# Optimization experiments

Hardware: AMD Instinct MI355X
Metric: run time of the kernel (lower is better)

The kernel has to match this reference:

```python
import jax, jax.numpy as jnp
import numpy as np

B, IN, H, O, L, G = 4096, 512, 1024, 256, 2, 3


def _lin_init(key, out_dim, in_dim):
    k1, k2 = jax.random.split(key)
    bound = 1.0 / np.sqrt(in_dim)
    w = jax.random.uniform(k1, (out_dim, in_dim), jnp.float32, -bound, bound)
    b = jax.random.uniform(k2, (out_dim,), jnp.float32, -bound, bound)
    return w, b


def setup_inputs() -> dict:
    key = jax.random.key(0)
    ks = jax.random.split(key, 10)
    x = jax.random.normal(ks[0], (B, IN), jnp.float32)
    hidden = jax.random.normal(ks[1], (L, B, H), jnp.float32)
    i2d_w, i2d_b = _lin_init(ks[2], H, IN)
    # stacked GRU params, PyTorch gate order (r, z, n); layer0 input dim == H (after i2d)
    kih = jax.random.split(ks[3], L)
    khh = jax.random.split(ks[4], L)
    gru_w_ih = jnp.stack([_lin_init(kih[l], 3 * H, H)[0] for l in range(L)])
    gru_b_ih = jnp.stack([_lin_init(kih[l], 3 * H, H)[1] for l in range(L)])
    gru_w_hh = jnp.stack([_lin_init(khh[l], 3 * H, H)[0] for l in range(L)])
    gru_b_hh = jnp.stack([_lin_init(khh[l], 3 * H, H)[1] for l in range(L)])
    mu_w, mu_b = _lin_init(ks[5], O * G, H)
    sigma_w, sigma_b = _lin_init(ks[6], O * G, H)
    pi_w, pi_b = _lin_init(ks[7], O * G, H)
    return {"x": x, "hidden": hidden, "i2d_w": i2d_w, "i2d_b": i2d_b,
            "gru_w_ih": gru_w_ih, "gru_w_hh": gru_w_hh,
            "gru_b_ih": gru_b_ih, "gru_b_hh": gru_b_hh,
            "mu_w": mu_w, "mu_b": mu_b, "sigma_w": sigma_w, "sigma_b": sigma_b,
            "pi_w": pi_w, "pi_b": pi_b, "batch_size": B}


def reference(x, hidden, i2d_w, i2d_b, gru_w_ih, gru_w_hh, gru_b_ih, gru_b_hh,
              mu_w, mu_b, sigma_w, sigma_b, pi_w, pi_b, batch_size):
    # input projection + relu
    h1 = jax.nn.relu(x @ i2d_w.T + i2d_b)  # [B, H]
    # single-timestep stacked GRU (PyTorch cell math, gate order r,z,n)
    inp = h1
    new_h = []
    for l in range(hidden.shape[0]):
        h_prev = hidden[l]
        gi = inp @ gru_w_ih[l].T + gru_b_ih[l]   # [B, 3H]
        gh = h_prev @ gru_w_hh[l].T + gru_b_hh[l]
        i_r, i_z, i_n = jnp.split(gi, 3, axis=-1)
        h_r, h_z, h_n = jnp.split(gh, 3, axis=-1)
        r = jax.nn.sigmoid(i_r + h_r)
        z = jax.nn.sigmoid(i_z + h_z)
        n = jnp.tanh(i_n + r * h_n)
        h_new = (1.0 - z) * n + z * h_prev
        new_h.append(h_new)
        inp = h_new
    hidden_out = jnp.stack(new_h)            # [L, B, H]
    h_out = jnp.tanh(inp)                    # [B, H]
    n_g = 3
    o = mu_w.shape[0] // n_g
    pi = jax.nn.softmax((h_out @ pi_w.T + pi_b).reshape(-1, n_g, o), axis=1)
    mu = (h_out @ mu_w.T + mu_b).reshape(-1, n_g, o)
    sig = jax.nn.softplus(h_out @ sigma_w.T + sigma_b).reshape(-1, n_g, o)
    return (mu, sig, pi, hidden_out)
```

## Files before the change

### kernel.cpp

```cpp
#include <hip/hip_runtime.h>
#include <stdint.h>

typedef unsigned short bf16u;
typedef float f32x4 __attribute__((ext_vector_type(4)));
typedef short bf16x8 __attribute__((ext_vector_type(8)));
typedef float f4 __attribute__((ext_vector_type(4)));

#define AS1 __attribute__((address_space(1)))
#define AS3 __attribute__((address_space(3)))

__device__ __forceinline__ float b2f(bf16u u) {
  union { uint32_t i; float f; } v; v.i = ((uint32_t)u) << 16; return v.f;
}
__device__ __forceinline__ uint32_t f2b(float f) {
  union { float f; uint32_t i; } v; v.f = f;
  uint32_t i = v.i;
  return (i + 0x7FFFu + ((i >> 16) & 1u)) >> 16;
}
__device__ __forceinline__ float sigm(float x) { return 1.f / (1.f + __expf(-x)); }
__device__ __forceinline__ float ftanh(float x) {
  float e = __expf(2.f * x);
  return 1.f - 2.f / (e + 1.f);
}
__device__ __forceinline__ uint4 pack8(f4 a, f4 b) {
  uint4 o;
  o.x = (f2b(a[0]) & 0xffffu) | (f2b(a[1]) << 16);
  o.y = (f2b(a[2]) & 0xffffu) | (f2b(a[3]) << 16);
  o.z = (f2b(b[0]) & 0xffffu) | (f2b(b[1]) << 16);
  o.w = (f2b(b[2]) & 0xffffu) | (f2b(b[3]) << 16);
  return o;
}

struct CvtSeg { const float* src; char* dst; int blk0; int count; int tobf16; };
struct CvtArgs { CvtSeg s[12]; int nseg; };

__global__ __launch_bounds__(256)
void cvt_multi(CvtArgs a) {
  int b = blockIdx.x, seg = 0;
  while (seg + 1 < a.nseg && b >= a.s[seg + 1].blk0) ++seg;
  const CvtSeg& S = a.s[seg];
  size_t idx = ((size_t)(b - S.blk0) * 2048) + (size_t)threadIdx.x * 8;
  if ((long long)idx >= S.count) return;
  f4 x = *(const f4*)&S.src[idx];
  f4 y = *(const f4*)&S.src[idx + 4];
  if (S.tobf16) {
    *(uint4*)((bf16u*)S.dst + idx) = pack8(x, y);
  } else {
    *(f4*)((float*)S.dst + idx) = x;
    *(f4*)((float*)S.dst + idx + 4) = y;
  }
}

__global__ __launch_bounds__(256)
void gemm_i2d(const float* __restrict__ xf, const bf16u* __restrict__ W,
              const float* __restrict__ bias, bf16u* __restrict__ Cout) {
  constexpr int K = 512, N = 1024;
  __shared__ bf16u sA[64 * 64];
  __shared__ bf16u sB[128 * 64];
  const int tid = threadIdx.x, wave = tid >> 6, lane = tid & 63;
  const int bn = blockIdx.x, bm = blockIdx.y;

  const int srA = wave * 16 + (lane >> 3);
  const int srB = wave * 32 + (lane >> 3);
  const int kc  = (lane & 7) ^ ((lane >> 3) & 7);
  const float* gx = xf + (size_t)(bm * 64 + srA) * K + kc * 8;
  const bf16u* wg = W + (size_t)(bn * 128 + srB) * K + kc * 8;
  const int adst = srA * 64 + (lane & 7) * 8;

  const int wm = wave >> 1, wn = wave & 1;
  const int q = lane >> 4, cl = lane & 15;

  int aoff[2][2], boff[4][2];
#pragma unroll
  for (int i = 0; i < 2; ++i) {
    int m = wm * 32 + i * 16 + cl;
#pragma unroll
    for (int kk = 0; kk < 2; ++kk)
      aoff[i][kk] = m * 64 + (((q + kk * 4) ^ (m & 7)) * 8);
  }
#pragma unroll
  for (int j = 0; j < 4; ++j) {
    int n = wn * 64 + j * 16 + cl;
#pragma unroll
    for (int kk = 0; kk < 2; ++kk)
      boff[j][kk] = n * 64 + (((q + kk * 4) ^ (n & 7)) * 8);
  }

  f32x4 acc[2][4] = {};
  for (int k0 = 0; k0 < K; k0 += 64) {
    f4 a0 = *(const f4*)(gx + k0);
    f4 a1 = *(const f4*)(gx + k0 + 4);
    f4 a2 = *(const f4*)(gx + (size_t)8 * K + k0);
    f4 a3 = *(const f4*)(gx + (size_t)8 * K + k0 + 4);
#pragma unroll
    for (int t = 0; t < 4; ++t)
      __builtin_amdgcn_global_load_lds(
          (const AS1 void*)(wg + k0 + (size_t)t * 8 * K),
          (AS3 void*)&sB[wave * 2048 + t * 512], 16, 0, 0);
    *(uint4*)&sA[adst]       = pack8(a0, a1);
    *(uint4*)&sA[adst + 512] = pack8(a2, a3);
    __syncthreads();
#pragma unroll
    for (int kk = 0; kk < 2; ++kk) {
      bf16x8 af[2], bfr[4];
#pragma unroll
      for (int i = 0; i < 2; ++i) af[i] = *(const bf16x8*)&sA[aoff[i][kk]];
#pragma unroll
      for (int j = 0; j < 4; ++j) bfr[j] = *(const bf16x8*)&sB[boff[j][kk]];
#pragma unroll
      for (int i = 0; i < 2; ++i)
#pragma unroll
        for (int j = 0; j < 4; ++j)
          acc[i][j] = __builtin_amdgcn_mfma_f32_16x16x32_bf16(af[i], bfr[j], acc[i][j], 0, 0, 0);
    }
    __syncthreads();
  }

  float bv[4];
#pragma unroll
  for (int j = 0; j < 4; ++j)
    bv[j] = bias[bn * 128 + wn * 64 + j * 16 + cl];

  const int row0 = bm * 64 + wm * 32 + q * 4;
  const int col0 = bn * 128 + wn * 64 + cl;
#pragma unroll
  for (int i = 0; i < 2; ++i)
#pragma unroll
    for (int j = 0; j < 4; ++j)
#pragma unroll
      for (int r = 0; r < 4; ++r) {
        float v = fmaxf(acc[i][j][r] + bv[j], 0.f);
        Cout[(size_t)(row0 + i * 16 + r) * N + (col0 + j * 16)] = (bf16u)f2b(v);
      }
}

template <int LAST>
__global__ __launch_bounds__(512)
void gru_fused(const bf16u* __restrict__ inp, const bf16u* __restrict__ hpb,
               const bf16u* __restrict__ wih, const bf16u* __restrict__ whh,
               const float* __restrict__ bih, const float* __restrict__ bhh,
               const float* __restrict__ hpf, float* __restrict__ hid_out,
               bf16u* __restrict__ nxt) {
  constexpr int K = 1024;
  __shared__ bf16u s[640 * 64];
  const int tid  = threadIdx.x;
  const int wave = tid >> 6;
  const int lane = tid & 63;
  const int bn = blockIdx.x, bm = blockIdx.y;
  const int c0 = bn * 64;

  const int rr  = tid >> 3;
  const int kc  = (tid & 7) ^ (rr & 7);
  const int dst0 = rr * 64 + (tid & 7) * 8;
  const bf16u* gI = inp + (size_t)(bm * 128 + rr) * K + kc * 8;
  const bf16u* gH = hpb + (size_t)(bm * 128 + rr) * K + kc * 8;
  const bf16u* gW[6];
#pragma unroll
  for (int p = 0; p < 6; ++p) {
    const bf16u* base = (p < 3) ? wih : whh;
    gW[p] = base + (size_t)((p % 3) * 1024 + c0 + rr) * K + kc * 8;
  }

  const int wm = wave >> 1, wn = wave & 1;
  const int q = lane >> 4, cl = lane & 15;

  int aoff[2][2], boff[2][2];
#pragma unroll
  for (int i = 0; i < 2; ++i) {
    int ai = wm * 32 + i * 16 + cl;
#pragma unroll
    for (int kk = 0; kk < 2; ++kk)
      aoff[i][kk] = ai * 64 + (((q + kk * 4) ^ (ai & 7)) * 8);
  }
#pragma unroll
  for (int j = 0; j < 2; ++j) {
    int br = wn * 32 + j * 16 + cl;
#pragma unroll
    for (int kk = 0; kk < 2; ++kk)
      boff[j][kk] = (256 + br) * 64 + (((q + kk * 4) ^ (br & 7)) * 8);
  }

  f32x4 acc[6][2][2] = {};

  for (int k0 = 0; k0 < K; k0 += 64) {
    __builtin_amdgcn_global_load_lds((const AS1 void*)(gI + k0),
        (AS3 void*)&s[dst0], 16, 0, 0);
    __builtin_amdgcn_global_load_lds((const AS1 void*)(gI + k0 + (size_t)64 * K),
        (AS3 void*)&s[dst0 + 4096], 16, 0, 0);
    __builtin_amdgcn_global_load_lds((const AS1 void*)(gH + k0),
        (AS3 void*)&s[dst0 + 8192], 16, 0, 0);
    __builtin_amdgcn_global_load_lds((const AS1 void*)(gH + k0 + (size_t)64 * K),
        (AS3 void*)&s[dst0 + 12288], 16, 0, 0);
#pragma unroll
    for (int p = 0; p < 6; ++p)
      __builtin_amdgcn_global_load_lds((const AS1 void*)(gW[p] + k0),
          (AS3 void*)&s[dst0 + (4 + p) * 4096], 16, 0, 0);
    __syncthreads();
#pragma unroll
    for (int kk = 0; kk < 2; ++kk) {
      bf16x8 aI[2], aH[2];
#pragma unroll
      for (int i = 0; i < 2; ++i) {
        aI[i] = *(const bf16x8*)&s[aoff[i][kk]];
        aH[i] = *(const bf16x8*)&s[aoff[i][kk] + 8192];
      }
#pragma unroll
      for (int p = 0; p < 6; ++p) {
        bf16x8 b0 = *(const bf16x8*)&s[boff[0][kk] + p * 4096];
        bf16x8 b1 = *(const bf16x8*)&s[boff[1][kk] + p * 4096];
        if (p < 3) {
          acc[p][0][0] = __builtin_amdgcn_mfma_f32_16x16x32_bf16(aI[0], b0, acc[p][0][0], 0, 0, 0);
          acc[p][0][1] = __builtin_amdgcn_mfma_f32_16x16x32_bf16(aI[0], b1, acc[p][0][1], 0, 0, 0);
          acc[p][1][0] = __builtin_amdgcn_mfma_f32_16x16x32_bf16(aI[1], b0, acc[p][1][0], 0, 0, 0);
          acc[p][1][1] = __builtin_amdgcn_mfma_f32_16x16x32_bf16(aI[1], b1, acc[p][1][1], 0, 0, 0);
        } else {
          acc[p][0][0] = __builtin_amdgcn_mfma_f32_16x16x32_bf16(aH[0], b0, acc[p][0][0], 0, 0, 0);
          acc[p][0][1] = __builtin_amdgcn_mfma_f32_16x16x32_bf16(aH[0], b1, acc[p][0][1], 0, 0, 0);
          acc[p][1][0] = __builtin_amdgcn_mfma_f32_16x16x32_bf16(aH[1], b0, acc[p][1][0], 0, 0, 0);
          acc[p][1][1] = __builtin_amdgcn_mfma_f32_16x16x32_bf16(aH[1], b1, acc[p][1][1], 0, 0, 0);
        }
      }
    }
    __syncthreads();
  }

  float bI[3][2], bH[3][2];
#pragma unroll
  for (int g = 0; g < 3; ++g)
#pragma unroll
    for (int j = 0; j < 2; ++j) {
      int col = c0 + wn * 32 + j * 16 + cl;
      bI[g][j] = bih[g * 1024 + col];
      bH[g][j] = bhh[g * 1024 + col];
    }

#pragma unroll
  for (int i = 0; i < 2; ++i)
#pragma unroll
    for (int j = 0; j < 2; ++j)
#pragma unroll
      for (int r_ = 0; r_ < 4; ++r_) {
        int row = bm * 128 + wm * 32 + i * 16 + q * 4 + r_;
        int col = c0 + wn * 32 + j * 16 + cl;
        size_t o = (size_t)row * 1024 + col;
        float vir = acc[0][i][j][r_] + bI[0][j];
        float viz = acc[1][i][j][r_] + bI[1][j];
        float vin = acc[2][i][j][r_] + bI[2][j];
        float vhr = acc[3][i][j][r_] + bH[0][j];
        float vhz = acc[4][i][j][r_] + bH[1][j];
        float vhn = acc[5][i][j][r_] + bH[2][j];
        float rg = sigm(vir + vhr);
        float zg = sigm(viz + vhz);
        float ng = ftanh(vin + rg * vhn);
        float hnew = (1.f - zg) * ng + zg * hpf[o];
        hid_out[o] = hnew;
        nxt[o] = (bf16u)f2b(LAST ? ftanh(hnew) : hnew);
      }
}

__global__ __launch_bounds__(256)
void gemm_heads2(const bf16u* __restrict__ A, const bf16u* __restrict__ Wp,
                 const float* __restrict__ biasp, float* __restrict__ out_mu,
                 float* __restrict__ out_sg, float* __restrict__ out_pi) {
  constexpr int K = 1024;
  __shared__ bf16u sA[64 * 64];
  __shared__ bf16u sB[192 * 64];
  const int tid = threadIdx.x, wave = tid >> 6, lane = tid & 63;
  const int bn = blockIdx.x, bm = blockIdx.y;
  const bool ispi = (bn >= 12);
  const int o0 = (bn - 12) * 64;
  const int nbt = ispi ? 6 : 4;

  const int srA = wave * 16 + (lane >> 3);
  const int kc  = (lane & 7) ^ ((lane >> 3) & 7);
  const bf16u* ag = A + (size_t)(bm * 64 + srA) * K + kc * 8;
  const bf16u* wg[6];
#pragma unroll
  for (int t = 0; t < 6; ++t) {
    int wrow;
    if (!ispi) wrow = bn * 128 + t * 32 + wave * 8 + (lane >> 3);
    else       wrow = 1536 + (t >> 1) * 256 + o0 + (t & 1) * 32 + wave * 8 + (lane >> 3);
    wg[t] = Wp + (size_t)wrow * K + kc * 8;
  }

  const int wm = wave >> 1, wn = wave & 1;
  const int q = lane >> 4, cl = lane & 15;

  int aoff[2][2], boff[6][2];
#pragma unroll
  for (int i = 0; i < 2; ++i) {
    int m = wm * 32 + i * 16 + cl;
#pragma unroll
    for (int kk = 0; kk < 2; ++kk)
      aoff[i][kk] = m * 64 + (((q + kk * 4) ^ (m & 7)) * 8);
  }
#pragma unroll
  for (int j = 0; j < 6; ++j) {
    int l = ispi ? ((j >> 1) * 64 + wn * 32 + (j & 1) * 16 + cl)
                 : (wn * 64 + (j & 3) * 16 + cl);
#pragma unroll
    for (int kk = 0; kk < 2; ++kk)
      boff[j][kk] = l * 64 + (((q + kk * 4) ^ (l & 7)) * 8);
  }

  f32x4 acc[2][6] = {};
  for (int k0 = 0; k0 < K; k0 += 64) {
#pragma unroll
    for (int t = 0; t < 2; ++t)
      __builtin_amdgcn_global_load_lds(
          (const AS1 void*)(ag + k0 + (size_t)t * 8 * K),
          (AS3 void*)&sA[wave * 1024 + t * 512], 16, 0, 0);
#pragma unroll
    for (int t = 0; t < 6; ++t)
      if (t < nbt)
        __builtin_amdgcn_global_load_lds(
            (const AS1 void*)(wg[t] + k0),
            (AS3 void*)&sB[t * 2048 + wave * 512], 16, 0, 0);
    __syncthreads();
#pragma unroll
    for (int kk = 0; kk < 2; ++kk) {
      bf16x8 af[2];
#pragma unroll
      for (int i = 0; i < 2; ++i) af[i] = *(const bf16x8*)&sA[aoff[i][kk]];
#pragma unroll
      for (int j = 0; j < 6; ++j) {
        if (j >= nbt) continue;
        bf16x8 bf_ = *(const bf16x8*)&sB[boff[j][kk]];
#pragma unroll
        for (int i = 0; i < 2; ++i)
          acc[i][j] = __builtin_amdgcn_mfma_f32_16x16x32_bf16(af[i], bf_, acc[i][j], 0, 0, 0);
      }
    }
    __syncthreads();
  }

  const int row0 = bm * 64 + wm * 32 + q * 4;
  if (!ispi) {
    float bv[4];
#pragma unroll
    for (int j = 0; j < 4; ++j)
      bv[j] = biasp[bn * 128 + wn * 64 + j * 16 + cl];
    const int head = bn / 6;
    const int ch0 = (bn % 6) * 128 + wn * 64 + cl;
#pragma unroll
    for (int i = 0; i < 2; ++i)
#pragma unroll
      for (int j = 0; j < 4; ++j)
#pragma unroll
        for (int r = 0; r < 4; ++r) {
          float v = acc[i][j][r] + bv[j];
          size_t off = (size_t)(row0 + i * 16 + r) * 768 + (ch0 + j * 16);
          if (head == 0) out_mu[off] = v;
          else out_sg[off] = fmaxf(v, 0.f) + __logf(1.f + __expf(-fabsf(v)));
        }
  } else {
    float bv[6];
#pragma unroll
    for (int j = 0; j < 6; ++j)
      bv[j] = biasp[1536 + (j >> 1) * 256 + o0 + wn * 32 + (j & 1) * 16 + cl];
#pragma unroll
    for (int i = 0; i < 2; ++i)
#pragma unroll
      for (int jo = 0; jo < 2; ++jo)
#pragma unroll
        for (int r = 0; r < 4; ++r) {
          float v0 = acc[i][jo][r]     + bv[jo];
          float v1 = acc[i][2 + jo][r] + bv[2 + jo];
          float v2 = acc[i][4 + jo][r] + bv[4 + jo];
          float m = fmaxf(fmaxf(v0, v1), v2);
          float e0 = __expf(v0 - m), e1 = __expf(v1 - m), e2 = __expf(v2 - m);
          float sc = 1.f / (e0 + e1 + e2);
          size_t base = (size_t)(row0 + i * 16 + r) * 768
                        + (o0 + wn * 32 + jo * 16 + cl);
          out_pi[base]       = e0 * sc;
          out_pi[base + 256] = e1 * sc;
          out_pi[base + 512] = e2 * sc;
        }
  }
}

extern "C" void kernel_launch(void* const* d_in, const int* in_sizes, int n_in,
                              void* d_out, int out_size, void* d_ws, size_t ws_size,
                              hipStream_t stream) {
  const float* x      = (const float*)d_in[0];
  const float* hidden = (const float*)d_in[1];
  const float* i2d_w  = (const float*)d_in[2];
  const float* i2d_b  = (const float*)d_in[3];
  const float* w_ih   = (const float*)d_in[4];
  const float* w_hh   = (const float*)d_in[5];
  const float* b_ih   = (const float*)d_in[6];
  const float* b_hh   = (const float*)d_in[7];
  const float* mu_w   = (const float*)d_in[8];
  const float* mu_b   = (const float*)d_in[9];
  const float* sg_w   = (const float*)d_in[10];
  const float* sg_b   = (const float*)d_in[11];
  const float* pi_w   = (const float*)d_in[12];
  const float* pi_b   = (const float*)d_in[13];
  float* out = (float*)d_out;

  const size_t BH = 4194304;
  const int HS = 3145728;
  float* hid_base = out + (size_t)3 * HS;

  dim3 blk(256, 1, 1);

  bf16u* wb_i2d = (bf16u*)d_ws;
  bf16u* wb_ih  = wb_i2d + 524288;
  bf16u* wb_hh  = wb_ih + 6291456;
  bf16u* wb_hd  = wb_hh + 6291456;
  float* biasp  = (float*)((char*)d_ws + 30932992);
  const size_t wbytes = 30942208;

  {
    CvtArgs a{};
    int nb = 0;
    auto seg = [&](const float* s, void* d, int count, int tobf) {
      a.s[a.nseg++] = {s, (char*)d, nb, count, tobf};
      nb += (count + 2047) / 2048;
    };
    seg(i2d_w, wb_i2d, 524288, 1);
    seg(w_ih,  wb_ih, 6291456, 1);
    seg(w_hh,  wb_hh, 6291456, 1);
    seg(mu_w,  wb_hd, 786432, 1);
    seg(sg_w,  wb_hd + 786432, 786432, 1);
    seg(pi_w,  wb_hd + 1572864, 786432, 1);
    seg(mu_b,  biasp, 768, 0);
    seg(sg_b,  biasp + 768, 768, 0);
    seg(pi_b,  biasp + 1536, 768, 0);
    cvt_multi<<<dim3(nb), blk, 0, stream>>>(a);
  }

  int Bc = 4096;
  while (wbytes + (size_t)Bc * 8192 > ws_size && Bc > 256) Bc >>= 1;
  const int nchunk = 4096 / Bc;

  char* cbase = (char*)d_ws + wbytes;
  bf16u* ws0  = (bf16u*)cbase;
  bf16u* nxt0 = (bf16u*)(cbase + (size_t)Bc * 2048);
  bf16u* hb0  = (bf16u*)(cbase + (size_t)Bc * 4096);
  bf16u* hb1  = (bf16u*)(cbase + (size_t)Bc * 6144);

  for (int c = 0; c < nchunk; ++c) {
    const size_t off = (size_t)c * Bc;
    const float* h0_c = hidden + off * 1024;
    const float* h1_c = hidden + BH + off * 1024;

    {
      CvtArgs a{};
      int nb = 0;
      auto seg = [&](const float* s, void* d, int count) {
        a.s[a.nseg++] = {s, (char*)d, nb, count, 1};
        nb += (count + 2047) / 2048;
      };
      seg(h0_c, hb0, Bc * 1024);
      seg(h1_c, hb1, Bc * 1024);
      cvt_multi<<<dim3(nb), blk, 0, stream>>>(a);
    }

    gemm_i2d<<<dim3(8, Bc / 64), blk, 0, stream>>>(
        x + off * 512, wb_i2d, i2d_b, ws0);
    gru_fused<0><<<dim3(16, Bc / 128), dim3(512, 1, 1), 0, stream>>>(
        ws0, hb0, wb_ih, wb_hh, b_ih, b_hh, h0_c, hid_base + off * 1024, nxt0);
    gru_fused<1><<<dim3(16, Bc / 128), dim3(512, 1, 1), 0, stream>>>(
        nxt0, hb1, wb_ih + 3145728, wb_hh + 3145728, b_ih + 3072, b_hh + 3072,
        h1_c, hid_base + BH + off * 1024, ws0);
    gemm_heads2<<<dim3(16, Bc / 64), blk, 0, stream>>>(
        ws0, wb_hd, biasp, out + off * 768, out + HS + off * 768,
        out + 2 * (size_t)HS + off * 768);
  }
}
```

Measured before the change: 367.2 us.

## Merge hidden-state conversion into weight conversion and widen heads GEMM tile

The hidden-state fp32-to-bf16 conversion is folded into the single upfront weight conversion launch, so it is no longer a separate per-chunk launch. The workspace layout is reorganized to hold the full bf16 hidden buffers. The heads GEMM now uses 512-thread blocks covering 128 rows with one shared LDS buffer, which halves the grid and lets each B tile be reused across more rows. The risks are larger LDS use per block, possible occupancy loss, and a bigger workspace requirement that may shrink the chunk size.

```diff
diff --git a/kernel.cpp b/kernel.cpp
--- a/kernel.cpp
+++ b/kernel.cpp
@@ -258,29 +258,28 @@
       }
 }
 
-__global__ __launch_bounds__(256)
-void gemm_heads2(const bf16u* __restrict__ A, const bf16u* __restrict__ Wp,
+__global__ __launch_bounds__(512)
+void gemm_heads3(const bf16u* __restrict__ A, const bf16u* __restrict__ Wp,
                  const float* __restrict__ biasp, float* __restrict__ out_mu,
                  float* __restrict__ out_sg, float* __restrict__ out_pi) {
   constexpr int K = 1024;
-  __shared__ bf16u sA[64 * 64];
-  __shared__ bf16u sB[192 * 64];
+  __shared__ bf16u s[320 * 64];
   const int tid = threadIdx.x, wave = tid >> 6, lane = tid & 63;
   const int bn = blockIdx.x, bm = blockIdx.y;
   const bool ispi = (bn >= 12);
   const int o0 = (bn - 12) * 64;
-  const int nbt = ispi ? 6 : 4;
-
-  const int srA = wave * 16 + (lane >> 3);
-  const int kc  = (lane & 7) ^ ((lane >> 3) & 7);
-  const bf16u* ag = A + (size_t)(bm * 64 + srA) * K + kc * 8;
-  const bf16u* wg[6];
-#pragma unroll
-  for (int t = 0; t < 6; ++t) {
-    int wrow;
-    if (!ispi) wrow = bn * 128 + t * 32 + wave * 8 + (lane >> 3);
-    else       wrow = 1536 + (t >> 1) * 256 + o0 + (t & 1) * 32 + wave * 8 + (lane >> 3);
-    wg[t] = Wp + (size_t)wrow * K + kc * 8;
+  const int nbt = ispi ? 3 : 2;
+  const int nj  = ispi ? 6 : 4;
+
+  const int rr  = tid >> 3;
+  const int kc  = (tid & 7) ^ (rr & 7);
+  const int dst0 = rr * 64 + (tid & 7) * 8;
+  const bf16u* gA = A + (size_t)(bm * 128 + rr) * K + kc * 8;
+  const bf16u* gB[3];
+#pragma unroll
+  for (int t = 0; t < 3; ++t) {
+    int wrow = ispi ? (1536 + t * 256 + o0 + rr) : (bn * 128 + t * 64 + rr);
+    gB[t] = Wp + (size_t)wrow * K + kc * 8;
   }
 
   const int wm = wave >> 1, wn = wave & 1;
@@ -300,32 +299,30 @@
                  : (wn * 64 + (j & 3) * 16 + cl);
 #pragma unroll
     for (int kk = 0; kk < 2; ++kk)
-      boff[j][kk] = l * 64 + (((q + kk * 4) ^ (l & 7)) * 8);
+      boff[j][kk] = 8192 + l * 64 + (((q + kk * 4) ^ (l & 7)) * 8);
   }
 
   f32x4 acc[2][6] = {};
   for (int k0 = 0; k0 < K; k0 += 64) {
-#pragma unroll
-    for (int t = 0; t < 2; ++t)
-      __builtin_amdgcn_global_load_lds(
-          (const AS1 void*)(ag + k0 + (size_t)t * 8 * K),
-          (AS3 void*)&sA[wave * 1024 + t * 512], 16, 0, 0);
-#pragma unroll
-    for (int t = 0; t < 6; ++t)
+    __builtin_amdgcn_global_load_lds((const AS1 void*)(gA + k0),
+        (AS3 void*)&s[dst0], 16, 0, 0);
+    __builtin_amdgcn_global_load_lds((const AS1 void*)(gA + k0 + (size_t)64 * K),
+        (AS3 void*)&s[dst0 + 4096], 16, 0, 0);
+#pragma unroll
+    for (int t = 0; t < 3; ++t)
       if (t < nbt)
-        __builtin_amdgcn_global_load_lds(
-            (const AS1 void*)(wg[t] + k0),
-            (AS3 void*)&sB[t * 2048 + wave * 512], 16, 0, 0);
+        __builtin_amdgcn_global_load_lds((const AS1 void*)(gB[t] + k0),
+            (AS3 void*)&s[8192 + dst0 + t * 4096], 16, 0, 0);
     __syncthreads();
 #pragma unroll
     for (int kk = 0; kk < 2; ++kk) {
       bf16x8 af[2];
 #pragma unroll
-      for (int i = 0; i < 2; ++i) af[i] = *(const bf16x8*)&sA[aoff[i][kk]];
+      for (int i = 0; i < 2; ++i) af[i] = *(const bf16x8*)&s[aoff[i][kk]];
 #pragma unroll
       for (int j = 0; j < 6; ++j) {
-        if (j >= nbt) continue;
-        bf16x8 bf_ = *(const bf16x8*)&sB[boff[j][kk]];
+        if (j >= nj) continue;
+        bf16x8 bf_ = *(const bf16x8*)&s[boff[j][kk]];
 #pragma unroll
         for (int i = 0; i < 2; ++i)
           acc[i][j] = __builtin_amdgcn_mfma_f32_16x16x32_bf16(af[i], bf_, acc[i][j], 0, 0, 0);
@@ -334,7 +331,7 @@
     __syncthreads();
   }
 
-  const int row0 = bm * 64 + wm * 32 + q * 4;
+  const int row0 = bm * 128 + wm * 32 + q * 4;
   if (!ispi) {
     float bv[4];
 #pragma unroll
@@ -411,6 +408,10 @@
   float* biasp  = (float*)((char*)d_ws + 30932992);
   const size_t wbytes = 30942208;
 
+  bf16u* hb0 = (bf16u*)((char*)d_ws + wbytes);
+  bf16u* hb1 = hb0 + BH;
+  const size_t hbbytes = (size_t)2 * BH * 2;
+
   {
     CvtArgs a{};
     int nb = 0;
@@ -427,44 +428,32 @@
     seg(mu_b,  biasp, 768, 0);
     seg(sg_b,  biasp + 768, 768, 0);
     seg(pi_b,  biasp + 1536, 768, 0);
+    seg(hidden, hb0, 8388608, 1);
     cvt_multi<<<dim3(nb), blk, 0, stream>>>(a);
   }
 
   int Bc = 4096;
-  while (wbytes + (size_t)Bc * 8192 > ws_size && Bc > 256) Bc >>= 1;
+  while (wbytes + hbbytes + (size_t)Bc * 4096 > ws_size && Bc > 256) Bc >>= 1;
   const int nchunk = 4096 / Bc;
 
-  char* cbase = (char*)d_ws + wbytes;
+  char* cbase = (char*)d_ws + wbytes + hbbytes;
   bf16u* ws0  = (bf16u*)cbase;
   bf16u* nxt0 = (bf16u*)(cbase + (size_t)Bc * 2048);
-  bf16u* hb0  = (bf16u*)(cbase + (size_t)Bc * 4096);
-  bf16u* hb1  = (bf16u*)(cbase + (size_t)Bc * 6144);
 
   for (int c = 0; c < nchunk; ++c) {
     const size_t off = (size_t)c * Bc;
     const float* h0_c = hidden + off * 1024;
     const float* h1_c = hidden + BH + off * 1024;
 
-    {
-      CvtArgs a{};
-      int nb = 0;
-      auto seg = [&](const float* s, void* d, int count) {
-        a.s[a.nseg++] = {s, (char*)d, nb, count, 1};
-        nb += (count + 2047) / 2048;
-      };
-      seg(h0_c, hb0, Bc * 1024);
-      seg(h1_c, hb1, Bc * 1024);
-      cvt_multi<<<dim3(nb), blk, 0, stream>>>(a);
-    }
-
     gemm_i2d<<<dim3(8, Bc / 64), blk, 0, stream>>>(
         x + off * 512, wb_i2d, i2d_b, ws0);
     gru_fused<0><<<dim3(16, Bc / 128), dim3(512, 1, 1), 0, stream>>>(
-        ws0, hb0, wb_ih, wb_hh, b_ih, b_hh, h0_c, hid_base + off * 1024, nxt0);
+        ws0, hb0 + off * 1024, wb_ih, wb_hh, b_ih, b_hh, h0_c,
+        hid_base + off * 1024, nxt0);
     gru_fused<1><<<dim3(16, Bc / 128), dim3(512, 1, 1), 0, stream>>>(
-        nxt0, hb1, wb_ih + 3145728, wb_hh + 3145728, b_ih + 3072, b_hh + 3072,
-        h1_c, hid_base + BH + off * 1024, ws0);
-    gemm_heads2<<<dim3(16, Bc / 64), blk, 0, stream>>>(
+        nxt0, hb1 + off * 1024, wb_ih + 3145728, wb_hh + 3145728,
+        b_ih + 3072, b_hh + 3072, h1_c, hid_base + BH + off * 1024, ws0);
+    gemm_heads3<<<dim3(16, Bc / 128), dim3(512, 1, 1), 0, stream>>>(
         ws0, wb_hd, biasp, out + off * 768, out + HS + off * 768,
         out + 2 * (size_t)HS + off * 768);
   }
```

Result: no change. 360.7 us (-1.8%).
